# Optimization experiments

Measured on AMD Instinct MI355X. Metric: run time of the kernel, lower is better.

## Reference

```python
import jax, jax.numpy as jnp
import numpy as np

# Ragged per-mixture-component spectral sample counts (static allocation).
COUNTS = [150, 120, 100, 90, 80, 60]
OFFSETS = np.concatenate([[0], np.cumsum(COUNTS)])  # [0,150,270,370,460,540,600]
TWO_PI = 2.0 * np.pi


def setup_inputs() -> dict:
    key = jax.random.key(0)
    k_x, k_w, k_mu, k_std, k_eps = jax.random.split(key, 5)
    N, D, Q = 100000, 8, 6
    S = int(OFFSETS[-1])
    x = jax.random.normal(k_x, (N, D), dtype=jnp.float32)
    # weight/std are positive (they come from Param.transform() in the original)
    weight = jax.random.uniform(k_w, (Q,), dtype=jnp.float32, minval=0.1, maxval=1.0)
    mu = jax.random.normal(k_mu, (Q, D), dtype=jnp.float32)
    std = jax.random.uniform(k_std, (Q, D), dtype=jnp.float32, minval=0.1, maxval=1.0)
    eps = jax.random.normal(k_eps, (S, D), dtype=jnp.float32)
    return {"x": x, "weight": weight, "mu": mu, "std": std, "eps": eps}


def reference(x, weight, mu, std, eps):
    # x: [N, D]; weight: [Q]; mu, std: [Q, D]; eps: [S, D] with S = sum(COUNTS)
    comp_idx = np.repeat(np.arange(len(COUNTS)), COUNTS)  # static [S]
    # spectral points: mu[i] + std[i] * eps  (per-component Gaussian samples)
    spectral = mu[comp_idx] + std[comp_idx] * eps          # [S, D]
    xdot = TWO_PI * (x @ spectral.T)                       # [N, S]
    c, s = jnp.cos(xdot), jnp.sin(xdot)
    pieces = []
    for i, cnt in enumerate(COUNTS):
        sc = jnp.sqrt(weight[i] / cnt)
        lo, hi = int(OFFSETS[i]), int(OFFSETS[i + 1])
        # per-component [cos_i, sin_i] ordering, as in the torch loop
        pieces.append(sc * c[:, lo:hi])
        pieces.append(sc * s[:, lo:hi])
    return jnp.concatenate(pieces, axis=1)  # [N, 2*S]
```

## Files before the change

### kernel.cpp

```cpp
#include <hip/hip_runtime.h>
#include <math.h>

typedef float v2f __attribute__((ext_vector_type(2)));
typedef float v4f __attribute__((ext_vector_type(4)));

constexpr int D      = 8;
constexpr int S_TOT  = 600;
constexpr int PAIRS  = 300;
constexpr int BLOCK  = 320;
constexpr int RPB    = 50;
constexpr int ROW_F  = 2 * S_TOT;

__global__ __launch_bounds__(BLOCK) void ssgpr_rep_sm_kernel(
    const float* __restrict__ x,
    const float* __restrict__ weight,
    const float* __restrict__ mu,
    const float* __restrict__ stdv,
    const float* __restrict__ eps,
    float* __restrict__ out,
    int N)
{
    __shared__ float lbuf[2][ROW_F];

    const int p = (int)threadIdx.x;
    const bool owner = (p < PAIRS);
    const int s0 = 2 * p;

    v2f W0{}, W1{}, W2{}, W3{}, W4{}, W5{}, W6{}, W7{};
    float sc = 0.f;
    int ccol = 0, scol = 0;
    if (owner) {
        const int offs[7] = {0, 150, 270, 370, 460, 540, 600};
        int i = 0;
        #pragma unroll
        for (int k = 1; k < 6; ++k) i += (s0 >= offs[k]);

        const float4* mu4 = reinterpret_cast<const float4*>(mu);
        const float4* sd4 = reinterpret_cast<const float4*>(stdv);
        const float4* ep4 = reinterpret_cast<const float4*>(eps);
        const float4 m0 = mu4[i * 2], m1 = mu4[i * 2 + 1];
        const float4 d0 = sd4[i * 2], d1 = sd4[i * 2 + 1];
        const float4 e0a = ep4[(size_t)s0 * 2],     e0b = ep4[(size_t)s0 * 2 + 1];
        const float4 e1a = ep4[(size_t)s0 * 2 + 2], e1b = ep4[(size_t)s0 * 2 + 3];

        W0 = (v2f){ m0.x + d0.x * e0a.x, m0.x + d0.x * e1a.x };
        W1 = (v2f){ m0.y + d0.y * e0a.y, m0.y + d0.y * e1a.y };
        W2 = (v2f){ m0.z + d0.z * e0a.z, m0.z + d0.z * e1a.z };
        W3 = (v2f){ m0.w + d0.w * e0a.w, m0.w + d0.w * e1a.w };
        W4 = (v2f){ m1.x + d1.x * e0b.x, m1.x + d1.x * e1b.x };
        W5 = (v2f){ m1.y + d1.y * e0b.y, m1.y + d1.y * e1b.y };
        W6 = (v2f){ m1.z + d1.z * e0b.z, m1.z + d1.z * e1b.z };
        W7 = (v2f){ m1.w + d1.w * e0b.w, m1.w + d1.w * e1b.w };

        sc   = sqrtf(weight[i] / (float)(offs[i + 1] - offs[i]));
        ccol = s0 + offs[i];
        scol = s0 + offs[i + 1];
    }

    const int n0 = (int)blockIdx.x * RPB;
    const int nrows = min(RPB, N - n0);

    for (int r = 0; r < nrows; ++r) {
        const int n   = n0 + r;
        const int buf = r & 1;

        if (owner) {
            const float4* xv = reinterpret_cast<const float4*>(x) + (size_t)n * 2;
            const float4 x0 = xv[0];
            const float4 x1 = xv[1];

            v2f acc = W0 * x0.x;
            acc += W1 * x0.y;  acc += W2 * x0.z;  acc += W3 * x0.w;
            acc += W4 * x1.x;  acc += W5 * x1.y;  acc += W6 * x1.z;
            acc += W7 * x1.w;

            float r0 = acc.x - floorf(acc.x);
            float r1 = acc.y - floorf(acc.y);
            v2f cpair = { sc * __builtin_amdgcn_cosf(r0),
                          sc * __builtin_amdgcn_cosf(r1) };
            v2f spair = { sc * __builtin_amdgcn_sinf(r0),
                          sc * __builtin_amdgcn_sinf(r1) };

            *reinterpret_cast<v2f*>(&lbuf[buf][ccol]) = cpair;
            *reinterpret_cast<v2f*>(&lbuf[buf][scol]) = spair;
        }
        __syncthreads();

        if (owner) {
            const v4f q = *reinterpret_cast<const v4f*>(&lbuf[buf][4 * p]);
            *reinterpret_cast<v4f*>(out + (size_t)n * ROW_F + 4 * p) = q;
        }
    }
}

extern "C" void kernel_launch(void* const* d_in, const int* in_sizes, int n_in,
                              void* d_out, int out_size, void* d_ws, size_t ws_size,
                              hipStream_t stream) {
    const float* x      = (const float*)d_in[0];
    const float* weight = (const float*)d_in[1];
    const float* mu     = (const float*)d_in[2];
    const float* stdv   = (const float*)d_in[3];
    const float* eps    = (const float*)d_in[4];
    float* out = (float*)d_out;

    const int N = in_sizes[0] / D;
    const int grid = (N + RPB - 1) / RPB;
    ssgpr_rep_sm_kernel<<<grid, BLOCK, 0, stream>>>(x, weight, mu, stdv, eps, out, N);
}
```

Baseline: 113.7 us.

## Write output columns directly per thread, expressing sine as a phase-shifted cosine

Each thread now owns four consecutive output columns. It builds a frequency vector for each column and, for sine columns, adds a -0.25 phase offset so that a single cosine covers both cos and sin. This removes the shared-memory staging buffer and the per-row __syncthreads. The cost is duplicated dot-product work, since each sample's projection is computed separately for its cos and sin columns, plus more registers holding four frequency vectors.

```diff
diff --git a/kernel.cpp b/kernel.cpp
--- a/kernel.cpp
+++ b/kernel.cpp
@@ -6,12 +6,12 @@
 
 constexpr int D      = 8;
 constexpr int S_TOT  = 600;
-constexpr int PAIRS  = 300;
+constexpr int QUADS  = 300;
 constexpr int BLOCK  = 320;
 constexpr int RPB    = 50;
 constexpr int ROW_F  = 2 * S_TOT;
 
-__global__ __launch_bounds__(BLOCK) void ssgpr_rep_sm_kernel(
+__global__ __launch_bounds__(BLOCK) void ssgpr_direct4_kernel(
     const float* __restrict__ x,
     const float* __restrict__ weight,
     const float* __restrict__ mu,
@@ -20,76 +20,82 @@
     float* __restrict__ out,
     int N)
 {
-    __shared__ float lbuf[2][ROW_F];
+    const int p = (int)threadIdx.x;
+    if (p >= QUADS) return;
 
-    const int p = (int)threadIdx.x;
-    const bool owner = (p < PAIRS);
-    const int s0 = 2 * p;
+    const int offs[7] = {0, 150, 270, 370, 460, 540, 600};
+    const int dofs[7] = {0, 300, 540, 740, 920, 1080, 1200};
+    const int c0 = 4 * p;
 
-    v2f W0{}, W1{}, W2{}, W3{}, W4{}, W5{}, W6{}, W7{};
-    float sc = 0.f;
-    int ccol = 0, scol = 0;
-    if (owner) {
-        const int offs[7] = {0, 150, 270, 370, 460, 540, 600};
-        int i = 0;
-        #pragma unroll
-        for (int k = 1; k < 6; ++k) i += (s0 >= offs[k]);
+    int i = 0;
+    #pragma unroll
+    for (int k = 1; k < 6; ++k) i += (c0 >= dofs[k]);
+    const int   cnt = offs[i + 1] - offs[i];
+    const float sc  = sqrtf(weight[i] / (float)cnt);
 
-        const float4* mu4 = reinterpret_cast<const float4*>(mu);
-        const float4* sd4 = reinterpret_cast<const float4*>(stdv);
-        const float4* ep4 = reinterpret_cast<const float4*>(eps);
-        const float4 m0 = mu4[i * 2], m1 = mu4[i * 2 + 1];
-        const float4 d0 = sd4[i * 2], d1 = sd4[i * 2 + 1];
-        const float4 e0a = ep4[(size_t)s0 * 2],     e0b = ep4[(size_t)s0 * 2 + 1];
-        const float4 e1a = ep4[(size_t)s0 * 2 + 2], e1b = ep4[(size_t)s0 * 2 + 3];
-
-        W0 = (v2f){ m0.x + d0.x * e0a.x, m0.x + d0.x * e1a.x };
-        W1 = (v2f){ m0.y + d0.y * e0a.y, m0.y + d0.y * e1a.y };
-        W2 = (v2f){ m0.z + d0.z * e0a.z, m0.z + d0.z * e1a.z };
-        W3 = (v2f){ m0.w + d0.w * e0a.w, m0.w + d0.w * e1a.w };
-        W4 = (v2f){ m1.x + d1.x * e0b.x, m1.x + d1.x * e1b.x };
-        W5 = (v2f){ m1.y + d1.y * e0b.y, m1.y + d1.y * e1b.y };
-        W6 = (v2f){ m1.z + d1.z * e0b.z, m1.z + d1.z * e1b.z };
-        W7 = (v2f){ m1.w + d1.w * e0b.w, m1.w + d1.w * e1b.w };
-
-        sc   = sqrtf(weight[i] / (float)(offs[i + 1] - offs[i]));
-        ccol = s0 + offs[i];
-        scol = s0 + offs[i + 1];
+    int   sj[4];
+    float ph[4];
+    #pragma unroll
+    for (int j = 0; j < 4; ++j) {
+        const int rel    = c0 + j - dofs[i];
+        const int is_sin = rel >= cnt;
+        sj[j] = offs[i] + rel - (is_sin ? cnt : 0);
+        ph[j] = is_sin ? -0.25f : 0.0f;
     }
 
-    const int n0 = (int)blockIdx.x * RPB;
+    const float4* mu4 = reinterpret_cast<const float4*>(mu) + i * 2;
+    const float4* sd4 = reinterpret_cast<const float4*>(stdv) + i * 2;
+    const float4* ep4 = reinterpret_cast<const float4*>(eps);
+    const float4 m0 = mu4[0], m1 = mu4[1];
+    const float4 d0 = sd4[0], d1 = sd4[1];
+    const float4 eA0 = ep4[2 * (size_t)sj[0]], eA1 = ep4[2 * (size_t)sj[0] + 1];
+    const float4 eB0 = ep4[2 * (size_t)sj[1]], eB1 = ep4[2 * (size_t)sj[1] + 1];
+    const float4 eC0 = ep4[2 * (size_t)sj[2]], eC1 = ep4[2 * (size_t)sj[2] + 1];
+    const float4 eD0 = ep4[2 * (size_t)sj[3]], eD1 = ep4[2 * (size_t)sj[3] + 1];
+
+    const float M[8]  = {m0.x, m0.y, m0.z, m0.w, m1.x, m1.y, m1.z, m1.w};
+    const float Sd[8] = {d0.x, d0.y, d0.z, d0.w, d1.x, d1.y, d1.z, d1.w};
+    const float EA[8] = {eA0.x, eA0.y, eA0.z, eA0.w, eA1.x, eA1.y, eA1.z, eA1.w};
+    const float EB[8] = {eB0.x, eB0.y, eB0.z, eB0.w, eB1.x, eB1.y, eB1.z, eB1.w};
+    const float EC[8] = {eC0.x, eC0.y, eC0.z, eC0.w, eC1.x, eC1.y, eC1.z, eC1.w};
+    const float ED[8] = {eD0.x, eD0.y, eD0.z, eD0.w, eD1.x, eD1.y, eD1.z, eD1.w};
+
+    v2f Wa[8], Wb[8];
+    #pragma unroll
+    for (int d = 0; d < 8; ++d) {
+        Wa[d] = (v2f){ M[d] + Sd[d] * EA[d], M[d] + Sd[d] * EB[d] };
+        Wb[d] = (v2f){ M[d] + Sd[d] * EC[d], M[d] + Sd[d] * ED[d] };
+    }
+    const v2f ph01 = {ph[0], ph[1]};
+    const v2f ph23 = {ph[2], ph[3]};
+
+    const int n0    = (int)blockIdx.x * RPB;
     const int nrows = min(RPB, N - n0);
+    const float* xp = x + (size_t)n0 * D;
+    float*       op = out + (size_t)n0 * ROW_F + c0;
 
     for (int r = 0; r < nrows; ++r) {
-        const int n   = n0 + r;
-        const int buf = r & 1;
+        const float4 x0 = *reinterpret_cast<const float4*>(xp);
+        const float4 x1 = *reinterpret_cast<const float4*>(xp + 4);
+        const float xs[8] = {x0.x, x0.y, x0.z, x0.w, x1.x, x1.y, x1.z, x1.w};
 
-        if (owner) {
-            const float4* xv = reinterpret_cast<const float4*>(x) + (size_t)n * 2;
-            const float4 x0 = xv[0];
-            const float4 x1 = xv[1];
+        v2f a = ph01, b = ph23;
+        #pragma unroll
+        for (int d = 0; d < 8; ++d) { a += Wa[d] * xs[d]; b += Wb[d] * xs[d]; }
 
-            v2f acc = W0 * x0.x;
-            acc += W1 * x0.y;  acc += W2 * x0.z;  acc += W3 * x0.w;
-            acc += W4 * x1.x;  acc += W5 * x1.y;  acc += W6 * x1.z;
-            acc += W7 * x1.w;
+        const float r0 = a.x - floorf(a.x);
+        const float r1 = a.y - floorf(a.y);
+        const float r2 = b.x - floorf(b.x);
+        const float r3 = b.y - floorf(b.y);
 
-            float r0 = acc.x - floorf(acc.x);
-            float r1 = acc.y - floorf(acc.y);
-            v2f cpair = { sc * __builtin_amdgcn_cosf(r0),
-                          sc * __builtin_amdgcn_cosf(r1) };
-            v2f spair = { sc * __builtin_amdgcn_sinf(r0),
-                          sc * __builtin_amdgcn_sinf(r1) };
+        const v4f q = { sc * __builtin_amdgcn_cosf(r0),
+                        sc * __builtin_amdgcn_cosf(r1),
+                        sc * __builtin_amdgcn_cosf(r2),
+                        sc * __builtin_amdgcn_cosf(r3) };
+        *reinterpret_cast<v4f*>(op) = q;
 
-            *reinterpret_cast<v2f*>(&lbuf[buf][ccol]) = cpair;
-            *reinterpret_cast<v2f*>(&lbuf[buf][scol]) = spair;
-        }
-        __syncthreads();
-
-        if (owner) {
-            const v4f q = *reinterpret_cast<const v4f*>(&lbuf[buf][4 * p]);
-            *reinterpret_cast<v4f*>(out + (size_t)n * ROW_F + 4 * p) = q;
-        }
+        xp += D;
+        op += ROW_F;
     }
 }
 
@@ -105,5 +111,5 @@
 
     const int N = in_sizes[0] / D;
     const int grid = (N + RPB - 1) / RPB;
-    ssgpr_rep_sm_kernel<<<grid, BLOCK, 0, stream>>>(x, weight, mu, stdv, eps, out, N);
+    ssgpr_direct4_kernel<<<grid, BLOCK, 0, stream>>>(x, weight, mu, stdv, eps, out, N);
 }
```

After: 115.3 us. No clear change (+1.5%).
